# Performance work log

Hardware: AMD Instinct MI355X
Metric: run time of the kernel (lower is better)

Reference implementation:

```python
import jax, jax.numpy as jnp
import numpy as np

B, S, D, H, DFF = 2, 2048, 1024, 16, 4096
DK = D // H
EPS = 1e-6


def setup_inputs() -> dict:
    key = jax.random.key(0)
    ks = jax.random.split(key, 16)
    sd = 0.02
    inp = {
        "x": jax.random.normal(ks[0], (B, S, D), jnp.float32),
        "mask": jnp.zeros((1, 1, S, S), jnp.float32),
        "wq": jax.random.normal(ks[1], (D, D), jnp.float32) * sd,
        "bq": jnp.zeros((D,), jnp.float32),
        "wk": jax.random.normal(ks[2], (D, D), jnp.float32) * sd,
        "bk": jnp.zeros((D,), jnp.float32),
        "wv": jax.random.normal(ks[3], (D, D), jnp.float32) * sd,
        "bv": jnp.zeros((D,), jnp.float32),
        "wo": jax.random.normal(ks[4], (D, D), jnp.float32) * sd,
        "bo": jnp.zeros((D,), jnp.float32),
        "w1": jax.random.normal(ks[5], (DFF, D), jnp.float32) * sd,
        "b1": jnp.zeros((DFF,), jnp.float32),
        "w2": jax.random.normal(ks[6], (D, DFF), jnp.float32) * sd,
        "b2": jnp.zeros((D,), jnp.float32),
        "alpha": jnp.ones((1,), jnp.float32),
        "gamma": jnp.zeros((1,), jnp.float32),
    }
    return inp


def _layer_norm(x, alpha, gamma):
    mean = jnp.mean(x, axis=-1, keepdims=True)
    var = jnp.mean((x - mean) ** 2, axis=-1, keepdims=True)
    return alpha * (x - mean) / jnp.sqrt(var + EPS) + gamma


def reference(x, mask, wq, bq, wk, bk, wv, bv, wo, bo, w1, b1, w2, b2, alpha, gamma):
    # --- multi-head attention (hand-rolled, full NxN scores) ---
    q = (x @ wq.T + bq).reshape(B, S, H, DK).transpose(0, 2, 1, 3)  # [B,H,S,DK]
    k = (x @ wk.T + bk).reshape(B, S, H, DK).transpose(0, 2, 1, 3)
    v = (x @ wv.T + bv).reshape(B, S, H, DK).transpose(0, 2, 1, 3)
    scores = jnp.einsum('bhqd,bhkd->bhqk', q, k) / np.sqrt(DK)  # [B,H,S,S]
    scores = scores + mask
    attn = jax.nn.softmax(scores, axis=-1)
    ctx = jnp.einsum('bhqk,bhkd->bhqd', attn, v)  # [B,H,S,DK]
    ctx = ctx.transpose(0, 2, 1, 3).reshape(B, S, D)
    attn_out = ctx @ wo.T + bo
    # residual + LayerNorm (dropout is identity in eval)
    out1 = _layer_norm(x + attn_out, alpha, gamma)
    # --- position-wise feed-forward ---
    ffn = jax.nn.relu(out1 @ w1.T + b1) @ w2.T + b2
    out2 = _layer_norm(out1 + ffn, alpha, gamma)
    return out2
```

## Files before the change

kernel.cpp:

```cpp
#include <hip/hip_runtime.h>


typedef float  f32x4   __attribute__((ext_vector_type(4)));
typedef float  f32x16  __attribute__((ext_vector_type(16)));
typedef __bf16 bf16x8  __attribute__((ext_vector_type(8)));
typedef __bf16 bf16x4  __attribute__((ext_vector_type(4)));

#define DEVI static __device__ __forceinline__

DEVI f32x4 mfma16(bf16x8 a, bf16x8 b, f32x4 c) {
    return __builtin_amdgcn_mfma_f32_16x16x32_bf16(a, b, c, 0, 0, 0);
}
DEVI f32x16 mfma32(bf16x8 a, bf16x8 b, f32x16 c) {
    return __builtin_amdgcn_mfma_f32_32x32x16_bf16(a, b, c, 0, 0, 0);
}

DEVI void gll16(const void* g, void* l) {
    __builtin_amdgcn_global_load_lds(
        (__attribute__((address_space(1))) void*)g,
        (__attribute__((address_space(3))) void*)l, 16, 0, 0);
}

DEVI __bf16 f2bf(float f) { return (__bf16)f; }

DEVI unsigned cvtpk_bf16(float a, float b) {
    unsigned d;
    asm("v_cvt_pk_bf16_f32 %0, %1, %2" : "=v"(d) : "v"(a), "v"(b));
    return d;
}
DEVI void permswap(unsigned& a, unsigned& b) {
    asm("v_permlane32_swap_b32 %0, %1" : "+v"(a), "+v"(b));
}
DEVI void permswapf(float& a, float& b) {
    asm("v_permlane32_swap_b32 %0, %1" : "+v"(a), "+v"(b));
}

__global__ void init_flag_kernel(int* f) { *f = 0; }

__global__ void mask_scan_kernel(const float* __restrict__ m, int* __restrict__ flag) {
    size_t i = (size_t)blockIdx.x * 256 + threadIdx.x;
    const float4* p = (const float4*)m;
    float4 a = p[i * 2], b = p[i * 2 + 1];
    bool nz = a.x != 0.f || a.y != 0.f || a.z != 0.f || a.w != 0.f ||
              b.x != 0.f || b.y != 0.f || b.z != 0.f || b.w != 0.f;
    if (__ballot(nz)) { if ((threadIdx.x & 63) == 0) atomicOr(flag, 1); }
}

__global__ void cast_bf16_kernel(const float* __restrict__ in, __bf16* __restrict__ out, int n8) {
    int i = blockIdx.x * 256 + threadIdx.x;
    if (i >= n8) return;
    const float4* p = (const float4*)in + (size_t)i * 2;
    float4 a = p[0], b = p[1];
    bf16x8 o = { (__bf16)a.x, (__bf16)a.y, (__bf16)a.z, (__bf16)a.w,
                 (__bf16)b.x, (__bf16)b.y, (__bf16)b.z, (__bf16)b.w };
    *(bf16x8*)(out + (size_t)i * 8) = o;
}

__global__ __launch_bounds__(256) void cast_weights_kernel(
    const float* __restrict__ wq, const float* __restrict__ wk,
    const float* __restrict__ wv, const float* __restrict__ wo,
    const float* __restrict__ w1, const float* __restrict__ w2,
    __bf16* __restrict__ wqb, __bf16* __restrict__ wkb,
    __bf16* __restrict__ wvb, __bf16* __restrict__ wob,
    __bf16* __restrict__ w1b, __bf16* __restrict__ w2b) {
    int i = blockIdx.x * 256 + threadIdx.x;
    const float* src; __bf16* dst; int off;
    if      (i <  131072) { src = wq; dst = wqb; off = i; }
    else if (i <  262144) { src = wk; dst = wkb; off = i -  131072; }
    else if (i <  393216) { src = wv; dst = wvb; off = i -  262144; }
    else if (i <  524288) { src = wo; dst = wob; off = i -  393216; }
    else if (i < 1048576) { src = w1; dst = w1b; off = i -  524288; }
    else                  { src = w2; dst = w2b; off = i - 1048576; }
    const float4* p = (const float4*)src + (size_t)off * 2;
    float4 a = p[0], b = p[1];
    bf16x8 o = { (__bf16)a.x, (__bf16)a.y, (__bf16)a.z, (__bf16)a.w,
                 (__bf16)b.x, (__bf16)b.y, (__bf16)b.z, (__bf16)b.w };
    *(bf16x8*)(dst + (size_t)off * 8) = o;
}

template <int YBF>
__global__ __launch_bounds__(256) void add_ln_kernel(
    const float* __restrict__ X, const void* __restrict__ Yv,
    const float* __restrict__ alphap, const float* __restrict__ gammap,
    float* __restrict__ outF, __bf16* __restrict__ outB) {
    const int tid = threadIdx.x, lane = tid & 63, wid = tid >> 6;
    const size_t base = (size_t)blockIdx.x * 1024 + tid * 4;
    float4 xv = *(const float4*)&X[base];
    float4 yv;
    if (YBF) {
        bf16x4 t = *(const bf16x4*)((const __bf16*)Yv + base);
        yv.x = (float)t[0]; yv.y = (float)t[1]; yv.z = (float)t[2]; yv.w = (float)t[3];
    } else {
        yv = *(const float4*)((const float*)Yv + base);
    }
    float vx = xv.x + yv.x, vy = xv.y + yv.y, vz = xv.z + yv.z, vw = xv.w + yv.w;
    float s = vx + vy + vz + vw;
    #pragma unroll
    for (int o = 32; o; o >>= 1) s += __shfl_xor(s, o);
    __shared__ float red[4];
    if (lane == 0) red[wid] = s;
    __syncthreads();
    float mean = (red[0] + red[1] + red[2] + red[3]) * (1.0f / 1024.0f);
    float dx = vx - mean, dy = vy - mean, dz = vz - mean, dw = vw - mean;
    float s2 = dx * dx + dy * dy + dz * dz + dw * dw;
    #pragma unroll
    for (int o = 32; o; o >>= 1) s2 += __shfl_xor(s2, o);
    __syncthreads();
    if (lane == 0) red[wid] = s2;
    __syncthreads();
    float var = (red[0] + red[1] + red[2] + red[3]) * (1.0f / 1024.0f);
    float rstd = rsqrtf(var + 1e-6f);
    float a = alphap[0], g = gammap[0];
    float4 o4 = { a * dx * rstd + g, a * dy * rstd + g, a * dz * rstd + g, a * dw * rstd + g };
    *(float4*)&outF[base] = o4;
    if (outB) {
        bf16x4 ob = { f2bf(o4.x), f2bf(o4.y), f2bf(o4.z), f2bf(o4.w) };
        *(bf16x4*)&outB[base] = ob;
    }
}

template <int N, int K, int BN, int MODE>
__global__ __launch_bounds__(256, 3) void gemm_bt_kernel(
    const __bf16* __restrict__ A, const __bf16* __restrict__ W,
    const float* __restrict__ bias, void* __restrict__ outp) {
    constexpr int WN = BN / 2;
    constexpr int NI = WN / 16;
    __shared__ __bf16 lsA[128 * 64];
    __shared__ __bf16 lsB[BN * 64];
    const int tid = threadIdx.x, wid = tid >> 6, lane = tid & 63;
    const int wr = wid >> 1, wc = wid & 1, l15 = lane & 15, hi = lane >> 4;
    const int m0 = blockIdx.y * 128, n0 = blockIdx.x * BN;
    f32x4 acc[4][NI] = {};
    for (int kt = 0; kt < K / 64; ++kt) {
        #pragma unroll
        for (int i = 0; i < 4; ++i) {
            int row = wid * 32 + i * 8 + (lane >> 3);
            gll16(A + (size_t)(m0 + row) * K + kt * 64 + ((lane & 7) ^ (row & 7)) * 8,
                  &lsA[(wid * 32 + i * 8) * 64]);
        }
        #pragma unroll
        for (int i = 0; i < BN / 32; ++i) {
            int row = wid * (BN / 4) + i * 8 + (lane >> 3);
            gll16(W + (size_t)(n0 + row) * K + kt * 64 + ((lane & 7) ^ (row & 7)) * 8,
                  &lsB[(wid * (BN / 4) + i * 8) * 64]);
        }
        __syncthreads();
        #pragma unroll
        for (int s = 0; s < 2; ++s) {
            bf16x8 af[4], bfv[NI];
            #pragma unroll
            for (int mi = 0; mi < 4; ++mi) {
                int row = wr * 64 + mi * 16 + l15;
                af[mi] = *(const bf16x8*)&lsA[row * 64 + (((s * 4 + hi) ^ (row & 7)) * 8)];
            }
            #pragma unroll
            for (int ni = 0; ni < NI; ++ni) {
                int row = wc * WN + ni * 16 + l15;
                bfv[ni] = *(const bf16x8*)&lsB[row * 64 + (((s * 4 + hi) ^ (row & 7)) * 8)];
            }
            #pragma unroll
            for (int mi = 0; mi < 4; ++mi)
                #pragma unroll
                for (int ni = 0; ni < NI; ++ni)
                    acc[mi][ni] = mfma16(af[mi], bfv[ni], acc[mi][ni]);
        }
        __syncthreads();
    }
    #pragma unroll
    for (int ni = 0; ni < NI; ++ni) {
        int col = n0 + wc * WN + ni * 16 + l15;
        float bv = bias[col];
        #pragma unroll
        for (int mi = 0; mi < 4; ++mi) {
            int rowb = m0 + wr * 64 + mi * 16 + hi * 4;
            #pragma unroll
            for (int r = 0; r < 4; ++r) {
                float v = acc[mi][ni][r] + bv;
                if (MODE == 0) {
                    ((float*)outp)[(size_t)(rowb + r) * N + col] = v;
                } else if (MODE == 1) {
                    v = fmaxf(v, 0.f);
                    ((__bf16*)outp)[(size_t)(rowb + r) * N + col] = f2bf(v);
                } else {
                    ((__bf16*)outp)[(size_t)(rowb + r) * N + col] = f2bf(v);
                }
            }
        }
    }
}

__global__ __launch_bounds__(256, 3) void gemm_qkv_kernel(
    const __bf16* __restrict__ A,
    const __bf16* __restrict__ wq, const __bf16* __restrict__ wk, const __bf16* __restrict__ wv,
    const float* __restrict__ bq, const float* __restrict__ bk, const float* __restrict__ bv,
    __bf16* __restrict__ q, __bf16* __restrict__ k, __bf16* __restrict__ vt) {
    constexpr int K = 1024;
    const int z = blockIdx.z;
    const __bf16* W = (z == 0) ? wq : (z == 1) ? wk : wv;
    const float* bias = (z == 0) ? bq : (z == 1) ? bk : bv;
    __shared__ __bf16 lsA[128 * 64];
    __shared__ __bf16 lsB[128 * 64];
    const int tid = threadIdx.x, wid = tid >> 6, lane = tid & 63;
    const int wr = wid >> 1, wc = wid & 1, l15 = lane & 15, hi = lane >> 4;
    const int m0 = blockIdx.y * 128, n0 = blockIdx.x * 128;
    f32x4 acc[4][4] = {};
    for (int kt = 0; kt < K / 64; ++kt) {
        #pragma unroll
        for (int i = 0; i < 4; ++i) {
            int row = wid * 32 + i * 8 + (lane >> 3);
            gll16(A + (size_t)(m0 + row) * K + kt * 64 + ((lane & 7) ^ (row & 7)) * 8,
                  &lsA[(wid * 32 + i * 8) * 64]);
            gll16(W + (size_t)(n0 + row) * K + kt * 64 + ((lane & 7) ^ (row & 7)) * 8,
                  &lsB[(wid * 32 + i * 8) * 64]);
        }
        __syncthreads();
        #pragma unroll
        for (int s = 0; s < 2; ++s) {
            bf16x8 af[4], bfv[4];
            #pragma unroll
            for (int mi = 0; mi < 4; ++mi) {
                int row = wr * 64 + mi * 16 + l15;
                af[mi] = *(const bf16x8*)&lsA[row * 64 + (((s * 4 + hi) ^ (row & 7)) * 8)];
            }
            #pragma unroll
            for (int ni = 0; ni < 4; ++ni) {
                int row = wc * 64 + ni * 16 + l15;
                bfv[ni] = *(const bf16x8*)&lsB[row * 64 + (((s * 4 + hi) ^ (row & 7)) * 8)];
            }
            #pragma unroll
            for (int mi = 0; mi < 4; ++mi)
                #pragma unroll
                for (int ni = 0; ni < 4; ++ni)
                    acc[mi][ni] = mfma16(af[mi], bfv[ni], acc[mi][ni]);
        }
        __syncthreads();
    }
    const float scale = (z == 0) ? 0.125f * 1.4426950408889634f : 1.0f;
    #pragma unroll
    for (int ni = 0; ni < 4; ++ni) {
        int col = n0 + wc * 64 + ni * 16 + l15;
        int h = col >> 6, dk = col & 63;
        float bvv = bias[col];
        #pragma unroll
        for (int mi = 0; mi < 4; ++mi) {
            int rowb = m0 + wr * 64 + mi * 16 + hi * 4;
            int b_ = rowb >> 11, sb = rowb & 2047;
            if (z < 2) {
                __bf16* dst = (z == 0) ? q : k;
                #pragma unroll
                for (int r = 0; r < 4; ++r)
                    dst[((size_t)(b_ * 16 + h) * 2048 + sb + r) * 64 + dk] =
                        f2bf((acc[mi][ni][r] + bvv) * scale);
            } else {
                bf16x4 o = { f2bf(acc[mi][ni][0] + bvv), f2bf(acc[mi][ni][1] + bvv),
                             f2bf(acc[mi][ni][2] + bvv), f2bf(acc[mi][ni][3] + bvv) };
                *(bf16x4*)&vt[((size_t)(b_ * 16 + h) * 64 + dk) * 2048 + sb] = o;
            }
        }
    }
}

__global__ __launch_bounds__(256, 2) void flash_attn_kernel(
    const __bf16* __restrict__ Q, const __bf16* __restrict__ Kx,
    const __bf16* __restrict__ VT, const float* __restrict__ mask,
    const int* __restrict__ mflag, __bf16* __restrict__ ctx) {
    __shared__ __bf16 Kl[2][64 * 64];
    __shared__ __bf16 Vl[2][64 * 64];
    const int lane = threadIdx.x & 63, wid = threadIdx.x >> 6;
    const int l31 = lane & 31, h = lane >> 5;
    const int id = blockIdx.x;
    const int xcd = id & 7, rest = id >> 3;
    const int qt = rest & 15;
    const int bh = (rest >> 4) * 8 + xcd;
    const int q0 = qt * 128 + wid * 32;

    bf16x8 qf[4];
    const size_t qrow = (size_t)bh * 2048 + q0 + l31;
    #pragma unroll
    for (int st = 0; st < 4; ++st)
        qf[st] = *(const bf16x8*)&Q[qrow * 64 + st * 16 + h * 8];

    const __bf16* kbase = Kx + (size_t)bh * 2048 * 64;
    const __bf16* vbase = VT + (size_t)bh * 64 * 2048;

    f32x16 c0 = {}, c1 = {};
    f32x16 lv = {};
    const bool useMask = (*mflag != 0);

    const int r0 = wid * 16;
    const int rA = r0 + (lane >> 3);
    const int rB = rA + 8;
    const int cA = (lane & 7) ^ (rA & 7);
    const int cB = (lane & 7) ^ (rB & 7);

    auto stage = [&](int b, int t) {
        gll16(kbase + (size_t)(t * 64 + rA) * 64 + cA * 8, &Kl[b][r0 * 64]);
        gll16(kbase + (size_t)(t * 64 + rB) * 64 + cB * 8, &Kl[b][(r0 + 8) * 64]);
        gll16(vbase + (size_t)rA * 2048 + t * 64 + cA * 8, &Vl[b][r0 * 64]);
        gll16(vbase + (size_t)rB * 2048 + t * 64 + cB * 8, &Vl[b][(r0 + 8) * 64]);
    };

    stage(0, 0);
    __syncthreads();
    int cur = 0;

    for (int t = 0; t < 32; ++t) {
        const int tn = (t + 1 < 32) ? t + 1 : t;
        stage(cur ^ 1, tn);
        #pragma unroll
        for (int s = 0; s < 2; ++s) {
            const int krow = s * 32 + l31;
            f32x16 sc = {};
            __builtin_amdgcn_s_setprio(1);
            #pragma unroll
            for (int st = 0; st < 4; ++st) {
                bf16x8 kf = *(const bf16x8*)&Kl[cur][krow * 64 + (((st * 2 + h) ^ (krow & 7)) * 8)];
                sc = mfma32(kf, qf[st], sc);
            }
            __builtin_amdgcn_s_setprio(0);
            if (useMask) {
                #pragma unroll
                for (int r = 0; r < 16; ++r) {
                    int kv = t * 64 + s * 32 + (r & 3) + 8 * (r >> 2) + 4 * h;
                    sc[r] += mask[(size_t)(q0 + l31) * 2048 + kv] * 1.4426950408889634f;
                }
            }
            #pragma unroll
            for (int r = 0; r < 16; ++r) sc[r] = exp2f(sc[r] - 40.0f);
            lv += sc;
            unsigned w0 = cvtpk_bf16(sc[0], sc[1]),   w2 = cvtpk_bf16(sc[4], sc[5]);
            unsigned w1 = cvtpk_bf16(sc[2], sc[3]),   w3 = cvtpk_bf16(sc[6], sc[7]);
            permswap(w0, w2); permswap(w1, w3);
            unsigned w4 = cvtpk_bf16(sc[8], sc[9]),   w6 = cvtpk_bf16(sc[12], sc[13]);
            unsigned w5 = cvtpk_bf16(sc[10], sc[11]), w7 = cvtpk_bf16(sc[14], sc[15]);
            permswap(w4, w6); permswap(w5, w7);
            uint4 u0 = { w0, w1, w2, w3 }, u1 = { w4, w5, w6, w7 };
            bf16x8 pb0, pb1;
            __builtin_memcpy(&pb0, &u0, 16);
            __builtin_memcpy(&pb1, &u1, 16);
            const int vr0 = l31, vr1 = 32 + l31;
            bf16x8 v00 = *(const bf16x8*)&Vl[cur][vr0 * 64 + (((s * 4 + 0 + h) ^ (vr0 & 7)) * 8)];
            bf16x8 v01 = *(const bf16x8*)&Vl[cur][vr0 * 64 + (((s * 4 + 2 + h) ^ (vr0 & 7)) * 8)];
            bf16x8 v10 = *(const bf16x8*)&Vl[cur][vr1 * 64 + (((s * 4 + 0 + h) ^ (vr1 & 7)) * 8)];
            bf16x8 v11 = *(const bf16x8*)&Vl[cur][vr1 * 64 + (((s * 4 + 2 + h) ^ (vr1 & 7)) * 8)];
            __builtin_amdgcn_s_setprio(1);
            c0 = mfma32(v00, pb0, c0);
            c0 = mfma32(v01, pb1, c0);
            c1 = mfma32(v10, pb0, c1);
            c1 = mfma32(v11, pb1, c1);
            __builtin_amdgcn_s_setprio(0);
        }
        __syncthreads();
        cur ^= 1;
    }

    float y8[8], y4[4];
    #pragma unroll
    for (int r = 0; r < 8; ++r) y8[r] = lv[2 * r] + lv[2 * r + 1];
    #pragma unroll
    for (int r = 0; r < 4; ++r) y4[r] = y8[2 * r] + y8[2 * r + 1];
    float ls = (y4[0] + y4[1]) + (y4[2] + y4[3]);
    float la = ls, lb = ls;
    permswapf(la, lb);
    const float rinv = 1.0f / (la + lb);

    const int b_ = bh >> 4, h_ = bh & 15;
    const size_t obase = ((size_t)b_ * 2048 + q0 + l31) * 1024 + (size_t)h_ * 64;
    #pragma unroll
    for (int g = 0; g < 4; ++g) {
        bf16x4 o0 = { f2bf(c0[4 * g + 0] * rinv), f2bf(c0[4 * g + 1] * rinv),
                      f2bf(c0[4 * g + 2] * rinv), f2bf(c0[4 * g + 3] * rinv) };
        *(bf16x4*)&ctx[obase + g * 8 + h * 4] = o0;
        bf16x4 o1 = { f2bf(c1[4 * g + 0] * rinv), f2bf(c1[4 * g + 1] * rinv),
                      f2bf(c1[4 * g + 2] * rinv), f2bf(c1[4 * g + 3] * rinv) };
        *(bf16x4*)&ctx[obase + 32 + g * 8 + h * 4] = o1;
    }
}

extern "C" void kernel_launch(void* const* d_in, const int* in_sizes, int n_in,
                              void* d_out, int out_size, void* d_ws, size_t ws_size,
                              hipStream_t stream) {
    const float* x     = (const float*)d_in[0];
    const float* mask  = (const float*)d_in[1];
    const float* wq    = (const float*)d_in[2];
    const float* bq    = (const float*)d_in[3];
    const float* wk    = (const float*)d_in[4];
    const float* bk    = (const float*)d_in[5];
    const float* wv    = (const float*)d_in[6];
    const float* bv    = (const float*)d_in[7];
    const float* wo    = (const float*)d_in[8];
    const float* bo    = (const float*)d_in[9];
    const float* w1    = (const float*)d_in[10];
    const float* b1    = (const float*)d_in[11];
    const float* w2    = (const float*)d_in[12];
    const float* b2    = (const float*)d_in[13];
    const float* alpha = (const float*)d_in[14];
    const float* gamma = (const float*)d_in[15];

    char* ws = (char*)d_ws;
    const size_t MB = 1u << 20;
    __bf16* xb    = (__bf16*)(ws + 0 * MB);
    __bf16* qb    = (__bf16*)(ws + 8 * MB);
    __bf16* kb    = (__bf16*)(ws + 16 * MB);
    __bf16* vtb   = (__bf16*)(ws + 24 * MB);
    __bf16* ctxb  = (__bf16*)(ws + 32 * MB);
    __bf16* wqb   = (__bf16*)(ws + 40 * MB);
    __bf16* wkb   = (__bf16*)(ws + 42 * MB);
    __bf16* wvb   = (__bf16*)(ws + 44 * MB);
    __bf16* wob   = (__bf16*)(ws + 46 * MB);
    __bf16* w1b   = (__bf16*)(ws + 48 * MB);
    __bf16* w2b   = (__bf16*)(ws + 56 * MB);
    __bf16* attnb = (__bf16*)(ws + 64 * MB);
    float*  out1  = (float*)(ws + 80 * MB);
    __bf16* out1b = (__bf16*)(ws + 96 * MB);
    __bf16* hid   = (__bf16*)(ws + 104 * MB);
    int*    mflag = (int*)(ws + 136 * MB);
    if (ws_size < 136 * MB + 64) return;

    init_flag_kernel<<<1, 1, 0, stream>>>(mflag);
    mask_scan_kernel<<<2048, 256, 0, stream>>>(mask, mflag);

    cast_bf16_kernel<<<2048, 256, 0, stream>>>(x, xb, 524288);
    cast_weights_kernel<<<6144, 256, 0, stream>>>(wq, wk, wv, wo, w1, w2,
                                                  wqb, wkb, wvb, wob, w1b, w2b);

    gemm_qkv_kernel<<<dim3(8, 32, 3), 256, 0, stream>>>(xb, wqb, wkb, wvb, bq, bk, bv,
                                                        qb, kb, vtb);
    flash_attn_kernel<<<dim3(512), 256, 0, stream>>>(qb, kb, vtb, mask, mflag, ctxb);
    gemm_bt_kernel<1024, 1024, 64, 2><<<dim3(16, 32), 256, 0, stream>>>(ctxb, wob, bo, attnb);
    add_ln_kernel<1><<<4096, 256, 0, stream>>>(x, attnb, alpha, gamma, out1, out1b);
    gemm_bt_kernel<4096, 1024, 128, 1><<<dim3(32, 32), 256, 0, stream>>>(out1b, w1b, b1, hid);
    gemm_bt_kernel<1024, 4096, 64, 2><<<dim3(16, 32), 256, 0, stream>>>(hid, w2b, b2, attnb);
    add_ln_kernel<1><<<4096, 256, 0, stream>>>(out1, attnb, alpha, gamma, (float*)d_out, nullptr);
}
```

Before: 262.2 us.

## Merge cast/mask-scan kernels and drop fp32 out1 round-trip

```diff
diff --git a/kernel.cpp b/kernel.cpp
--- a/kernel.cpp
+++ b/kernel.cpp
@@ -35,42 +35,35 @@
     asm("v_permlane32_swap_b32 %0, %1" : "+v"(a), "+v"(b));
 }
 
-__global__ void init_flag_kernel(int* f) { *f = 0; }
-
-__global__ void mask_scan_kernel(const float* __restrict__ m, int* __restrict__ flag) {
-    size_t i = (size_t)blockIdx.x * 256 + threadIdx.x;
-    const float4* p = (const float4*)m;
-    float4 a = p[i * 2], b = p[i * 2 + 1];
-    bool nz = a.x != 0.f || a.y != 0.f || a.z != 0.f || a.w != 0.f ||
-              b.x != 0.f || b.y != 0.f || b.z != 0.f || b.w != 0.f;
-    if (__ballot(nz)) { if ((threadIdx.x & 63) == 0) atomicOr(flag, 1); }
-}
-
-__global__ void cast_bf16_kernel(const float* __restrict__ in, __bf16* __restrict__ out, int n8) {
-    int i = blockIdx.x * 256 + threadIdx.x;
-    if (i >= n8) return;
-    const float4* p = (const float4*)in + (size_t)i * 2;
-    float4 a = p[0], b = p[1];
-    bf16x8 o = { (__bf16)a.x, (__bf16)a.y, (__bf16)a.z, (__bf16)a.w,
-                 (__bf16)b.x, (__bf16)b.y, (__bf16)b.z, (__bf16)b.w };
-    *(bf16x8*)(out + (size_t)i * 8) = o;
-}
-
-__global__ __launch_bounds__(256) void cast_weights_kernel(
+__global__ __launch_bounds__(256) void cast_all_kernel(
+    const float* __restrict__ x,
     const float* __restrict__ wq, const float* __restrict__ wk,
     const float* __restrict__ wv, const float* __restrict__ wo,
     const float* __restrict__ w1, const float* __restrict__ w2,
+    const float* __restrict__ mask,
+    __bf16* __restrict__ xb,
     __bf16* __restrict__ wqb, __bf16* __restrict__ wkb,
     __bf16* __restrict__ wvb, __bf16* __restrict__ wob,
-    __bf16* __restrict__ w1b, __bf16* __restrict__ w2b) {
+    __bf16* __restrict__ w1b, __bf16* __restrict__ w2b,
+    int* __restrict__ mflag) {
     int i = blockIdx.x * 256 + threadIdx.x;
+    if (i >= 2097152) {
+        int off = i - 2097152;
+        const float4* p = (const float4*)mask + (size_t)off * 2;
+        float4 a = p[0], b = p[1];
+        bool nz = a.x != 0.f || a.y != 0.f || a.z != 0.f || a.w != 0.f ||
+                  b.x != 0.f || b.y != 0.f || b.z != 0.f || b.w != 0.f;
+        if (__ballot(nz)) { if ((threadIdx.x & 63) == 0) atomicOr(mflag, 1); }
+        return;
+    }
     const float* src; __bf16* dst; int off;
-    if      (i <  131072) { src = wq; dst = wqb; off = i; }
-    else if (i <  262144) { src = wk; dst = wkb; off = i -  131072; }
-    else if (i <  393216) { src = wv; dst = wvb; off = i -  262144; }
-    else if (i <  524288) { src = wo; dst = wob; off = i -  393216; }
-    else if (i < 1048576) { src = w1; dst = w1b; off = i -  524288; }
-    else                  { src = w2; dst = w2b; off = i - 1048576; }
+    if      (i <  524288) { src = x;  dst = xb;  off = i; }
+    else if (i <  655360) { src = wq; dst = wqb; off = i -  524288; }
+    else if (i <  786432) { src = wk; dst = wkb; off = i -  655360; }
+    else if (i <  917504) { src = wv; dst = wvb; off = i -  786432; }
+    else if (i < 1048576) { src = wo; dst = wob; off = i -  917504; }
+    else if (i < 1572864) { src = w1; dst = w1b; off = i - 1048576; }
+    else                  { src = w2; dst = w2b; off = i - 1572864; }
     const float4* p = (const float4*)src + (size_t)off * 2;
     float4 a = p[0], b = p[1];
     bf16x8 o = { (__bf16)a.x, (__bf16)a.y, (__bf16)a.z, (__bf16)a.w,
@@ -78,15 +71,20 @@
     *(bf16x8*)(dst + (size_t)off * 8) = o;
 }
 
-template <int YBF>
+template <int XBF, int YBF>
 __global__ __launch_bounds__(256) void add_ln_kernel(
-    const float* __restrict__ X, const void* __restrict__ Yv,
+    const void* __restrict__ Xv, const void* __restrict__ Yv,
     const float* __restrict__ alphap, const float* __restrict__ gammap,
     float* __restrict__ outF, __bf16* __restrict__ outB) {
     const int tid = threadIdx.x, lane = tid & 63, wid = tid >> 6;
     const size_t base = (size_t)blockIdx.x * 1024 + tid * 4;
-    float4 xv = *(const float4*)&X[base];
-    float4 yv;
+    float4 xv, yv;
+    if (XBF) {
+        bf16x4 t = *(const bf16x4*)((const __bf16*)Xv + base);
+        xv.x = (float)t[0]; xv.y = (float)t[1]; xv.z = (float)t[2]; xv.w = (float)t[3];
+    } else {
+        xv = *(const float4*)((const float*)Xv + base);
+    }
     if (YBF) {
         bf16x4 t = *(const bf16x4*)((const __bf16*)Yv + base);
         yv.x = (float)t[0]; yv.y = (float)t[1]; yv.z = (float)t[2]; yv.w = (float)t[3];
@@ -112,7 +110,7 @@
     float rstd = rsqrtf(var + 1e-6f);
     float a = alphap[0], g = gammap[0];
     float4 o4 = { a * dx * rstd + g, a * dy * rstd + g, a * dz * rstd + g, a * dw * rstd + g };
-    *(float4*)&outF[base] = o4;
+    if (outF) *(float4*)&outF[base] = o4;
     if (outB) {
         bf16x4 ob = { f2bf(o4.x), f2bf(o4.y), f2bf(o4.z), f2bf(o4.w) };
         *(bf16x4*)&outB[base] = ob;
@@ -411,25 +409,22 @@
     __bf16* w1b   = (__bf16*)(ws + 48 * MB);
     __bf16* w2b   = (__bf16*)(ws + 56 * MB);
     __bf16* attnb = (__bf16*)(ws + 64 * MB);
-    float*  out1  = (float*)(ws + 80 * MB);
     __bf16* out1b = (__bf16*)(ws + 96 * MB);
     __bf16* hid   = (__bf16*)(ws + 104 * MB);
     int*    mflag = (int*)(ws + 136 * MB);
     if (ws_size < 136 * MB + 64) return;
 
-    init_flag_kernel<<<1, 1, 0, stream>>>(mflag);
-    mask_scan_kernel<<<2048, 256, 0, stream>>>(mask, mflag);
-
-    cast_bf16_kernel<<<2048, 256, 0, stream>>>(x, xb, 524288);
-    cast_weights_kernel<<<6144, 256, 0, stream>>>(wq, wk, wv, wo, w1, w2,
-                                                  wqb, wkb, wvb, wob, w1b, w2b);
+    hipMemsetAsync(mflag, 0, 4, stream);
+    cast_all_kernel<<<10240, 256, 0, stream>>>(x, wq, wk, wv, wo, w1, w2, mask,
+                                               xb, wqb, wkb, wvb, wob, w1b, w2b,
+                                               mflag);
 
     gemm_qkv_kernel<<<dim3(8, 32, 3), 256, 0, stream>>>(xb, wqb, wkb, wvb, bq, bk, bv,
                                                         qb, kb, vtb);
     flash_attn_kernel<<<dim3(512), 256, 0, stream>>>(qb, kb, vtb, mask, mflag, ctxb);
     gemm_bt_kernel<1024, 1024, 64, 2><<<dim3(16, 32), 256, 0, stream>>>(ctxb, wob, bo, attnb);
-    add_ln_kernel<1><<<4096, 256, 0, stream>>>(x, attnb, alpha, gamma, out1, out1b);
+    add_ln_kernel<0, 1><<<4096, 256, 0, stream>>>(x, attnb, alpha, gamma, nullptr, out1b);
     gemm_bt_kernel<4096, 1024, 128, 1><<<dim3(32, 32), 256, 0, stream>>>(out1b, w1b, b1, hid);
     gemm_bt_kernel<1024, 4096, 64, 2><<<dim3(16, 32), 256, 0, stream>>>(hid, w2b, b2, attnb);
-    add_ln_kernel<1><<<4096, 256, 0, stream>>>(out1, attnb, alpha, gamma, (float*)d_out, nullptr);
-}
+    add_ln_kernel<1, 1><<<4096, 256, 0, stream>>>(out1b, attnb, alpha, gamma, (float*)d_out, nullptr);
+}
```

After: 254.9 us, median of 2. -2.8%, faster.
